# Kernel tuning notes

Hardware: AMD Instinct MI355X
Metric: run time of the kernel (lower is better)

## Reference

```python
import jax, jax.numpy as jnp
import numpy as np

HEAD_SIZE = 64


def setup_inputs() -> dict:
    key = jax.random.key(0)
    kx, kk, kq, kv = jax.random.split(key, 4)
    B, T, C = 4, 4096, 1024
    x = jax.random.normal(kx, (B, T, C), dtype=jnp.float32)
    Wk = jax.random.normal(kk, (C, HEAD_SIZE), dtype=jnp.float32) * 0.02
    Wq = jax.random.normal(kq, (C, HEAD_SIZE), dtype=jnp.float32) * 0.02
    Wv = jax.random.normal(kv, (C, HEAD_SIZE), dtype=jnp.float32) * 0.02
    return {"x": x, "Wk": Wk, "Wq": Wq, "Wv": Wv}


def reference(x, Wk, Wq, Wv):
    # x: (B,T,C); projections to (B,T,H)
    T = x.shape[1]
    k = jnp.einsum('btc,ch->bth', x, Wk)
    q = jnp.einsum('btc,ch->bth', x, Wq)
    v = jnp.einsum('btc,ch->bth', x, Wv)
    scale = 1.0 / jnp.sqrt(jnp.float32(HEAD_SIZE))
    wei = jnp.einsum('bth,bsh->bts', q, k) * scale  # (B,T,T)
    causal = jnp.tril(jnp.ones((T, T), dtype=bool))
    wei = jnp.where(causal, wei, -jnp.inf)
    wei = jax.nn.softmax(wei, axis=-1)
    out = jnp.einsum('bts,bsh->bth', wei, v)  # (B,T,H)
    return out
```

## Files before the change

### kernel.cpp

```cpp
#include <hip/hip_runtime.h>

typedef __attribute__((ext_vector_type(8))) short short8;
typedef __attribute__((ext_vector_type(4))) float f32x4;
typedef unsigned short u16;

#define BB 4
#define TT 4096
#define CC 1024
#define HH 64

static __device__ __forceinline__ u16 f2bf(float f) {
    unsigned int u = __float_as_uint(f);
    unsigned int r = (u + 0x7FFFu + ((u >> 16) & 1u)) >> 16;
    return (u16)r;
}

static __device__ __forceinline__ int swz(int row, int chunk) {
    return row * 64 + ((chunk ^ (row & 7)) << 3);
}

__global__ void detect_dtype(const u16* __restrict__ xu, int* __restrict__ flag) {
    int lane = threadIdx.x;
    int cnt = 0;
    for (int i = lane; i < 1024; i += 64) {
        u16 u = xu[2 * i];
        int e = (u >> 7) & 0xFF;
        cnt += (e >= 100 && e <= 140) ? 1 : 0;
    }
    for (int d = 1; d < 64; d <<= 1) cnt += __shfl_xor(cnt, d);
    if (lane == 0) *flag = (cnt > 512) ? 1 : 0;
}

__global__ void wt_transpose(const void* __restrict__ Wk, const void* __restrict__ Wq,
                             const void* __restrict__ Wv, u16* __restrict__ Wtp,
                             const int* __restrict__ flag) {
    const int isbf = *flag;
    int r = blockIdx.x;
    int p = r >> 6;
    int n = r & 63;
    int nt = n >> 4, nl = n & 15;
    const void* W = (p == 0) ? Wq : (p == 1) ? Wk : Wv;
    int k0 = threadIdx.x * 4;
    int kb = k0 >> 6, k2 = (k0 >> 5) & 1, quad = (k0 >> 3) & 3, half = (k0 >> 2) & 1;
    ushort4 v;
    if (isbf) {
        const u16* Wb = (const u16*)W;
        v.x = Wb[(k0 + 0) * HH + n]; v.y = Wb[(k0 + 1) * HH + n];
        v.z = Wb[(k0 + 2) * HH + n]; v.w = Wb[(k0 + 3) * HH + n];
    } else {
        const float* Wf = (const float*)W;
        v.x = f2bf(Wf[(k0 + 0) * HH + n]); v.y = f2bf(Wf[(k0 + 1) * HH + n]);
        v.z = f2bf(Wf[(k0 + 2) * HH + n]); v.w = f2bf(Wf[(k0 + 3) * HH + n]);
    }
    size_t off16 = ((size_t)((p * 4 + nt) * 16 + kb) * 2 + k2) * 64 + quad * 16 + nl;
    *reinterpret_cast<ushort4*>(Wtp + off16 * 8 + half * 4) = v;
}

__global__ __launch_bounds__(256) void qkv_proj(const void* __restrict__ x,
                                                const u16* __restrict__ Wtp,
                                                u16* __restrict__ qo, u16* __restrict__ ko,
                                                u16* __restrict__ vo, const int* __restrict__ flag) {
    __shared__ __align__(16) u16 xs[16 * 1024];
    __shared__ __align__(16) u16 tls[4][3][256];
    const int isbf = *flag;
    const int tid = threadIdx.x;
    const int lane = tid & 63;
    const int w = tid >> 6;
    const int l15 = lane & 15;
    const int quad = lane >> 4;
    int phys = blockIdx.x;
    int rb = (phys & 7) * 128 + (phys >> 3);
    const int g0r = rb * 16;

    #pragma unroll
    for (int j = 0; j < 8; j++) {
        int c = tid + j * 256;
        int row = c >> 7, ck = c & 127;
        int dst = row * 1024 + ((ck ^ (row & 7)) << 3);
        if (isbf) {
            uint4 d = *reinterpret_cast<const uint4*>((const u16*)x + (size_t)(g0r + row) * CC + ck * 8);
            *reinterpret_cast<uint4*>(xs + dst) = d;
        } else {
            const float4* pf = reinterpret_cast<const float4*>((const float*)x + (size_t)(g0r + row) * CC + ck * 8);
            float4 a0 = pf[0], a1 = pf[1];
            ushort4 lo; lo.x = f2bf(a0.x); lo.y = f2bf(a0.y); lo.z = f2bf(a0.z); lo.w = f2bf(a0.w);
            ushort4 hi; hi.x = f2bf(a1.x); hi.y = f2bf(a1.y); hi.z = f2bf(a1.z); hi.w = f2bf(a1.w);
            *reinterpret_cast<ushort4*>(xs + dst) = lo;
            *reinterpret_cast<ushort4*>(xs + dst + 4) = hi;
        }
    }
    __syncthreads();

    f32x4 zero = {0.f, 0.f, 0.f, 0.f};
    f32x4 acc[3];
    #pragma unroll
    for (int i = 0; i < 3; i++) acc[i] = zero;

    for (int kb = 0; kb < 16; kb++) {
        #pragma unroll
        for (int k2 = 0; k2 < 2; k2++) {
            int ck = kb * 8 + k2 * 4 + quad;
            short8 af = *reinterpret_cast<const short8*>(xs + l15 * 1024 + ((ck ^ (l15 & 7)) << 3));
            #pragma unroll
            for (int p = 0; p < 3; p++) {
                short8 bf = *reinterpret_cast<const short8*>(
                    Wtp + ((((size_t)(p * 4 + w) * 16 + kb) * 2 + k2) * 64 + lane) * 8);
                acc[p] = __builtin_amdgcn_mfma_f32_16x16x32_bf16(af, bf, acc[p], 0, 0, 0);
            }
        }
    }

    const float qscale = 0.18033688011112042f;
    #pragma unroll
    for (int p = 0; p < 3; p++) {
        if (p < 2) {
            float sc = (p == 0) ? qscale : 1.f;
            #pragma unroll
            for (int r = 0; r < 4; r++)
                tls[w][p][(quad * 4 + r) * 16 + l15] = f2bf(acc[p][r] * sc);
        } else {
            #pragma unroll
            for (int r = 0; r < 4; r++)
                tls[w][p][l15 * 16 + quad * 4 + r] = f2bf(acc[p][r]);
        }
    }
    #pragma unroll
    for (int p = 0; p < 2; p++) {
        int t = lane >> 2, seg = lane & 3;
        ushort4 d = *reinterpret_cast<const ushort4*>(&tls[w][p][t * 16 + seg * 4]);
        u16* dst = (p == 0) ? qo : ko;
        *reinterpret_cast<ushort4*>(dst + (size_t)(g0r + t) * HH + w * 16 + seg * 4) = d;
    }
    {
        int c = lane >> 2, seg = lane & 3;
        ushort4 d = *reinterpret_cast<const ushort4*>(&tls[w][2][c * 16 + seg * 4]);
        int b = rb >> 8;
        int kt = (g0r & 4095) >> 6;
        int toff = g0r & 63;
        *reinterpret_cast<ushort4*>(vo + ((size_t)((b * 64 + kt) * 64 + w * 16 + c)) * 64 + toff + seg * 4) = d;
    }
}

__global__ __launch_bounds__(256) void attn(const u16* __restrict__ qp, const u16* __restrict__ kp,
                                            const u16* __restrict__ vp, float* __restrict__ acco,
                                            float* __restrict__ accl, void* __restrict__ outv,
                                            const int* __restrict__ flag, int nsplit) {
    __shared__ __align__(16) u16 kst[64 * 64];
    __shared__ __align__(16) u16 vts[64 * 64];
    __shared__ __align__(16) u16 pb[4][16 * 64];
    const int isbf = *flag;
    const int tid = threadIdx.x;
    const int lane = tid & 63;
    const int w = tid >> 6;
    const int l15 = lane & 15;
    const int quad = lane >> 4;

    int u = blockIdx.x;
    int b, qt, ks;
    if (nsplit == 1) {
        b = u >> 6;
        int raw = u & 63;
        qt = (raw & 1) ? (63 - (raw >> 1)) : (raw >> 1);
        ks = 0;
    } else {
        int per = 64 * nsplit;
        b = u / per;
        int rem = u - b * per;
        int i = rem / nsplit;
        qt = 63 - i;
        ks = rem - i * nsplit;
    }
    int qbase = qt * 64;
    int diag = qt;
    int nkt = diag + 1;
    if (ks >= nkt) return;

    short8 aq[2];
    {
        const u16* qrow = qp + (size_t)(b * TT + qbase + w * 16 + l15) * HH;
        aq[0] = *reinterpret_cast<const short8*>(qrow + quad * 8);
        aq[1] = *reinterpret_cast<const short8*>(qrow + 32 + quad * 8);
    }

    const int cc0 = tid, cc1 = tid + 256;
    const int dst0 = swz(cc0 >> 3, cc0 & 7);
    const int dst1 = swz(cc1 >> 3, cc1 & 7);
    const u16* kbase = kp + (size_t)b * TT * HH;
    const u16* vbase = vp + (size_t)b * 64 * 64 * 64;

    f32x4 zero = {0.f, 0.f, 0.f, 0.f};
    f32x4 o[4];
    #pragma unroll
    for (int i = 0; i < 4; i++) o[i] = zero;
    f32x4 lsum = zero;

    uint4 rk0 = *reinterpret_cast<const uint4*>(kbase + (size_t)ks * 4096 + cc0 * 8);
    uint4 rk1 = *reinterpret_cast<const uint4*>(kbase + (size_t)ks * 4096 + cc1 * 8);
    uint4 rv0 = *reinterpret_cast<const uint4*>(vbase + (size_t)ks * 4096 + cc0 * 8);
    uint4 rv1 = *reinterpret_cast<const uint4*>(vbase + (size_t)ks * 4096 + cc1 * 8);

    for (int kt = ks; kt < nkt; kt += nsplit) {
        __syncthreads();
        *reinterpret_cast<uint4*>(&kst[dst0]) = rk0;
        *reinterpret_cast<uint4*>(&kst[dst1]) = rk1;
        *reinterpret_cast<uint4*>(&vts[dst0]) = rv0;
        *reinterpret_cast<uint4*>(&vts[dst1]) = rv1;
        __syncthreads();
        int ktn = kt + nsplit;
        if (ktn < nkt) {
            rk0 = *reinterpret_cast<const uint4*>(kbase + (size_t)ktn * 4096 + cc0 * 8);
            rk1 = *reinterpret_cast<const uint4*>(kbase + (size_t)ktn * 4096 + cc1 * 8);
            rv0 = *reinterpret_cast<const uint4*>(vbase + (size_t)ktn * 4096 + cc0 * 8);
            rv1 = *reinterpret_cast<const uint4*>(vbase + (size_t)ktn * 4096 + cc1 * 8);
        }
        f32x4 s[4];
        #pragma unroll
        for (int i = 0; i < 4; i++) s[i] = zero;
        __builtin_amdgcn_s_setprio(1);
        #pragma unroll
        for (int k2 = 0; k2 < 2; k2++) {
            #pragma unroll
            for (int nt = 0; nt < 4; nt++) {
                short8 bf = *reinterpret_cast<const short8*>(&kst[swz(nt * 16 + l15, k2 * 4 + quad)]);
                s[nt] = __builtin_amdgcn_mfma_f32_16x16x32_bf16(aq[k2], bf, s[nt], 0, 0, 0);
            }
        }
        __builtin_amdgcn_s_setprio(0);
        const int rg = qbase + w * 16 + quad * 4;
        const bool dm = (kt == diag);
        #pragma unroll
        for (int nt = 0; nt < 4; nt++) {
            int key = kt * 64 + nt * 16 + l15;
            #pragma unroll
            for (int r = 0; r < 4; r++) {
                float p = __builtin_amdgcn_exp2f(s[nt][r]);
                if (dm && key > rg + r) p = 0.f;
                s[nt][r] = p;
            }
        }
        #pragma unroll
        for (int nt = 0; nt < 4; nt++) lsum = lsum + s[nt];
        #pragma unroll
        for (int nt = 0; nt < 4; nt++) {
            int chunk = nt * 2 + (l15 >> 3);
            int off = l15 & 7;
            #pragma unroll
            for (int r = 0; r < 4; r++) {
                int row = quad * 4 + r;
                pb[w][row * 64 + ((chunk ^ (row & 7)) << 3) + off] = f2bf(s[nt][r]);
            }
        }
        __builtin_amdgcn_s_setprio(1);
        #pragma unroll
        for (int k2 = 0; k2 < 2; k2++) {
            short8 ap = *reinterpret_cast<const short8*>(&pb[w][swz(l15, k2 * 4 + quad)]);
            #pragma unroll
            for (int nt = 0; nt < 4; nt++) {
                short8 bv = *reinterpret_cast<const short8*>(&vts[swz(nt * 16 + l15, k2 * 4 + quad)]);
                o[nt] = __builtin_amdgcn_mfma_f32_16x16x32_bf16(ap, bv, o[nt], 0, 0, 0);
            }
        }
        __builtin_amdgcn_s_setprio(0);
    }

    #pragma unroll
    for (int d = 1; d < 16; d <<= 1) {
        f32x4 t;
        #pragma unroll
        for (int r = 0; r < 4; r++) t[r] = __shfl_xor(lsum[r], d);
        lsum = lsum + t;
    }
    const int g0 = b * TT + qbase + w * 16 + quad * 4;

    if (nsplit == 1) {
        f32x4 inv;
        #pragma unroll
        for (int r = 0; r < 4; r++) inv[r] = 1.0f / lsum[r];
        if (isbf) {
            u16* outp = (u16*)outv;
            #pragma unroll
            for (int nt = 0; nt < 4; nt++)
                #pragma unroll
                for (int r = 0; r < 4; r++)
                    outp[(size_t)(g0 + r) * HH + nt * 16 + l15] = f2bf(o[nt][r] * inv[r]);
        } else {
            float* outp = (float*)outv;
            #pragma unroll
            for (int nt = 0; nt < 4; nt++)
                #pragma unroll
                for (int r = 0; r < 4; r++)
                    outp[(size_t)(g0 + r) * HH + nt * 16 + l15] = o[nt][r] * inv[r];
        }
    } else {
        float* accos = acco + (size_t)ks * (BB * TT * HH);
        float* accls = accl + (size_t)ks * (BB * TT);
        #pragma unroll
        for (int nt = 0; nt < 4; nt++)
            #pragma unroll
            for (int r = 0; r < 4; r++)
                accos[(size_t)(g0 + r) * HH + nt * 16 + l15] = o[nt][r];
        if (l15 == 0) {
            #pragma unroll
            for (int r = 0; r < 4; r++) accls[g0 + r] = lsum[r];
        }
    }
}

__global__ __launch_bounds__(256) void attn_finalize(const float* __restrict__ acco,
                                                     const float* __restrict__ accl,
                                                     void* __restrict__ outv,
                                                     const int* __restrict__ flag, int nsplit) {
    const int isbf = *flag;
    int i = blockIdx.x * blockDim.x + threadIdx.x;
    int row = i >> 4;
    int qt = (row & (TT - 1)) >> 6;
    int nact = min(nsplit, qt + 1);
    float4 ov = reinterpret_cast<const float4*>(acco)[i];
    float l = accl[row];
    for (int s = 1; s < nact; s++) {
        float4 t = reinterpret_cast<const float4*>(acco + (size_t)s * (BB * TT * HH))[i];
        ov.x += t.x; ov.y += t.y; ov.z += t.z; ov.w += t.w;
        l += accl[(size_t)s * (BB * TT) + row];
    }
    float inv = 1.0f / l;
    if (isbf) {
        ushort4 s;
        s.x = f2bf(ov.x * inv); s.y = f2bf(ov.y * inv);
        s.z = f2bf(ov.z * inv); s.w = f2bf(ov.w * inv);
        reinterpret_cast<ushort4*>(outv)[i] = s;
    } else {
        float4 s = {ov.x * inv, ov.y * inv, ov.z * inv, ov.w * inv};
        reinterpret_cast<float4*>(outv)[i] = s;
    }
}

extern "C" void kernel_launch(void* const* d_in, const int* in_sizes, int n_in,
                              void* d_out, int out_size, void* d_ws, size_t ws_size,
                              hipStream_t stream) {
    const void* x  = d_in[0];
    const void* Wk = d_in[1];
    const void* Wq = d_in[2];
    const void* Wv = d_in[3];
    char* ws = (char*)d_ws;
    u16* qo = (u16*)(ws);
    u16* ko = (u16*)(ws + (size_t)2 * 1024 * 1024);
    u16* vo = (u16*)(ws + (size_t)4 * 1024 * 1024);
    u16* Wtp = (u16*)(ws + (size_t)6 * 1024 * 1024);
    int* flag = (int*)(ws + (size_t)6 * 1024 * 1024 + 768 * 1024);
    float* acco = (float*)(ws + (size_t)7 * 1024 * 1024);
    float* accl = (float*)(ws + (size_t)39 * 1024 * 1024);

    const size_t need_split = (size_t)40 * 1024 * 1024;
    const int nsplit = (ws_size >= need_split) ? 8 : 1;

    detect_dtype<<<1, 64, 0, stream>>>((const u16*)x, flag);
    wt_transpose<<<192, 256, 0, stream>>>(Wk, Wq, Wv, Wtp, flag);
    qkv_proj<<<1024, 256, 0, stream>>>(x, Wtp, qo, ko, vo, flag);
    if (nsplit > 1) {
        attn<<<BB * 64 * nsplit, 256, 0, stream>>>(qo, ko, vo, acco, accl, d_out, flag, nsplit);
        attn_finalize<<<(BB * TT * HH / 4) / 256, 256, 0, stream>>>(acco, accl, d_out, flag, nsplit);
    } else {
        attn<<<BB * 64, 256, 0, stream>>>(qo, ko, vo, acco, accl, d_out, flag, 1);
    }
}
```

Baseline: 146.2 us.

## Fuse prep kernels, double rows per QKV block, merge split-K finalize into attention

Merges dtype detection and weight transpose into one prep kernel that also zeroes per-tile counters. The QKV projection block now handles 32 rows instead of 16, reusing each weight fragment for two MFMAs. The separate finalize launch is removed: the last split-K attention block for each query tile, found with an atomic counter, reduces the partials and writes the output. This cuts launch count and weight reloads, at the cost of doubled shared memory in qkv_proj and a serialized reduction tail inside attention.

```diff
diff --git a/kernel.cpp b/kernel.cpp
--- a/kernel.cpp
+++ b/kernel.cpp
@@ -19,8 +19,8 @@
     return row * 64 + ((chunk ^ (row & 7)) << 3);
 }
 
-__global__ void detect_dtype(const u16* __restrict__ xu, int* __restrict__ flag) {
-    int lane = threadIdx.x;
+static __device__ __forceinline__ int probe_isbf(const u16* xu, int tid) {
+    int lane = tid & 63;
     int cnt = 0;
     for (int i = lane; i < 1024; i += 64) {
         u16 u = xu[2 * i];
@@ -28,13 +28,26 @@
         cnt += (e >= 100 && e <= 140) ? 1 : 0;
     }
     for (int d = 1; d < 64; d <<= 1) cnt += __shfl_xor(cnt, d);
-    if (lane == 0) *flag = (cnt > 512) ? 1 : 0;
-}
-
-__global__ void wt_transpose(const void* __restrict__ Wk, const void* __restrict__ Wq,
-                             const void* __restrict__ Wv, u16* __restrict__ Wtp,
-                             const int* __restrict__ flag) {
-    const int isbf = *flag;
+    return (cnt > 512) ? 1 : 0;
+}
+
+__global__ void prep(const void* __restrict__ Wk, const void* __restrict__ Wq,
+                     const void* __restrict__ Wv, const u16* __restrict__ xu,
+                     u16* __restrict__ Wtp, int* __restrict__ flag, int* __restrict__ cnt) {
+    __shared__ int sflag;
+    if (threadIdx.x < 64) {
+        int f = probe_isbf(xu, threadIdx.x);
+        if (threadIdx.x == 0) sflag = f;
+    }
+    __syncthreads();
+    const int isbf = sflag;
+
+    if (blockIdx.x >= 192) {
+        if (threadIdx.x < 256) cnt[threadIdx.x] = 0;
+        if (threadIdx.x == 0) *flag = isbf;
+        return;
+    }
+
     int r = blockIdx.x;
     int p = r >> 6;
     int n = r & 63;
@@ -60,7 +73,7 @@
                                                 const u16* __restrict__ Wtp,
                                                 u16* __restrict__ qo, u16* __restrict__ ko,
                                                 u16* __restrict__ vo, const int* __restrict__ flag) {
-    __shared__ __align__(16) u16 xs[16 * 1024];
+    __shared__ __align__(16) u16 xs[32 * 1024];
     __shared__ __align__(16) u16 tls[4][3][256];
     const int isbf = *flag;
     const int tid = threadIdx.x;
@@ -69,11 +82,11 @@
     const int l15 = lane & 15;
     const int quad = lane >> 4;
     int phys = blockIdx.x;
-    int rb = (phys & 7) * 128 + (phys >> 3);
-    const int g0r = rb * 16;
-
-    #pragma unroll
-    for (int j = 0; j < 8; j++) {
+    int rb = (phys & 7) * 64 + (phys >> 3);
+    const int g0r = rb * 32;
+
+    #pragma unroll
+    for (int j = 0; j < 16; j++) {
         int c = tid + j * 256;
         int row = c >> 7, ck = c & 127;
         int dst = row * 1024 + ((ck ^ (row & 7)) << 3);
@@ -92,62 +105,71 @@
     __syncthreads();
 
     f32x4 zero = {0.f, 0.f, 0.f, 0.f};
-    f32x4 acc[3];
-    #pragma unroll
-    for (int i = 0; i < 3; i++) acc[i] = zero;
+    f32x4 acc[3][2];
+    #pragma unroll
+    for (int i = 0; i < 3; i++) { acc[i][0] = zero; acc[i][1] = zero; }
 
     for (int kb = 0; kb < 16; kb++) {
         #pragma unroll
         for (int k2 = 0; k2 < 2; k2++) {
             int ck = kb * 8 + k2 * 4 + quad;
-            short8 af = *reinterpret_cast<const short8*>(xs + l15 * 1024 + ((ck ^ (l15 & 7)) << 3));
+            int xo = ((ck ^ (l15 & 7)) << 3);
+            short8 af0 = *reinterpret_cast<const short8*>(xs + l15 * 1024 + xo);
+            short8 af1 = *reinterpret_cast<const short8*>(xs + (16 + l15) * 1024 + xo);
             #pragma unroll
             for (int p = 0; p < 3; p++) {
                 short8 bf = *reinterpret_cast<const short8*>(
                     Wtp + ((((size_t)(p * 4 + w) * 16 + kb) * 2 + k2) * 64 + lane) * 8);
-                acc[p] = __builtin_amdgcn_mfma_f32_16x16x32_bf16(af, bf, acc[p], 0, 0, 0);
+                acc[p][0] = __builtin_amdgcn_mfma_f32_16x16x32_bf16(af0, bf, acc[p][0], 0, 0, 0);
+                acc[p][1] = __builtin_amdgcn_mfma_f32_16x16x32_bf16(af1, bf, acc[p][1], 0, 0, 0);
             }
         }
     }
 
     const float qscale = 0.18033688011112042f;
     #pragma unroll
-    for (int p = 0; p < 3; p++) {
-        if (p < 2) {
-            float sc = (p == 0) ? qscale : 1.f;
-            #pragma unroll
-            for (int r = 0; r < 4; r++)
-                tls[w][p][(quad * 4 + r) * 16 + l15] = f2bf(acc[p][r] * sc);
-        } else {
-            #pragma unroll
-            for (int r = 0; r < 4; r++)
-                tls[w][p][l15 * 16 + quad * 4 + r] = f2bf(acc[p][r]);
-        }
-    }
-    #pragma unroll
-    for (int p = 0; p < 2; p++) {
-        int t = lane >> 2, seg = lane & 3;
-        ushort4 d = *reinterpret_cast<const ushort4*>(&tls[w][p][t * 16 + seg * 4]);
-        u16* dst = (p == 0) ? qo : ko;
-        *reinterpret_cast<ushort4*>(dst + (size_t)(g0r + t) * HH + w * 16 + seg * 4) = d;
-    }
-    {
-        int c = lane >> 2, seg = lane & 3;
-        ushort4 d = *reinterpret_cast<const ushort4*>(&tls[w][2][c * 16 + seg * 4]);
-        int b = rb >> 8;
-        int kt = (g0r & 4095) >> 6;
-        int toff = g0r & 63;
-        *reinterpret_cast<ushort4*>(vo + ((size_t)((b * 64 + kt) * 64 + w * 16 + c)) * 64 + toff + seg * 4) = d;
+    for (int rt = 0; rt < 2; rt++) {
+        const int g0rt = g0r + rt * 16;
+        #pragma unroll
+        for (int p = 0; p < 3; p++) {
+            if (p < 2) {
+                float sc = (p == 0) ? qscale : 1.f;
+                #pragma unroll
+                for (int r = 0; r < 4; r++)
+                    tls[w][p][(quad * 4 + r) * 16 + l15] = f2bf(acc[p][rt][r] * sc);
+            } else {
+                #pragma unroll
+                for (int r = 0; r < 4; r++)
+                    tls[w][p][l15 * 16 + quad * 4 + r] = f2bf(acc[p][rt][r]);
+            }
+        }
+        #pragma unroll
+        for (int p = 0; p < 2; p++) {
+            int t = lane >> 2, seg = lane & 3;
+            ushort4 d = *reinterpret_cast<const ushort4*>(&tls[w][p][t * 16 + seg * 4]);
+            u16* dst = (p == 0) ? qo : ko;
+            *reinterpret_cast<ushort4*>(dst + (size_t)(g0rt + t) * HH + w * 16 + seg * 4) = d;
+        }
+        {
+            int c = lane >> 2, seg = lane & 3;
+            ushort4 d = *reinterpret_cast<const ushort4*>(&tls[w][2][c * 16 + seg * 4]);
+            int b = g0rt >> 12;
+            int kt = (g0rt & 4095) >> 6;
+            int toff = g0rt & 63;
+            *reinterpret_cast<ushort4*>(vo + ((size_t)((b * 64 + kt) * 64 + w * 16 + c)) * 64 + toff + seg * 4) = d;
+        }
     }
 }
 
 __global__ __launch_bounds__(256) void attn(const u16* __restrict__ qp, const u16* __restrict__ kp,
                                             const u16* __restrict__ vp, float* __restrict__ acco,
                                             float* __restrict__ accl, void* __restrict__ outv,
-                                            const int* __restrict__ flag, int nsplit) {
+                                            const int* __restrict__ flag, int* __restrict__ cnt,
+                                            int nsplit) {
     __shared__ __align__(16) u16 kst[64 * 64];
     __shared__ __align__(16) u16 vts[64 * 64];
     __shared__ __align__(16) u16 pb[4][16 * 64];
+    __shared__ int is_last;
     const int isbf = *flag;
     const int tid = threadIdx.x;
     const int lane = tid & 63;
@@ -303,34 +325,37 @@
             #pragma unroll
             for (int r = 0; r < 4; r++) accls[g0 + r] = lsum[r];
         }
-    }
-}
-
-__global__ __launch_bounds__(256) void attn_finalize(const float* __restrict__ acco,
-                                                     const float* __restrict__ accl,
-                                                     void* __restrict__ outv,
-                                                     const int* __restrict__ flag, int nsplit) {
-    const int isbf = *flag;
-    int i = blockIdx.x * blockDim.x + threadIdx.x;
-    int row = i >> 4;
-    int qt = (row & (TT - 1)) >> 6;
-    int nact = min(nsplit, qt + 1);
-    float4 ov = reinterpret_cast<const float4*>(acco)[i];
-    float l = accl[row];
-    for (int s = 1; s < nact; s++) {
-        float4 t = reinterpret_cast<const float4*>(acco + (size_t)s * (BB * TT * HH))[i];
-        ov.x += t.x; ov.y += t.y; ov.z += t.z; ov.w += t.w;
-        l += accl[(size_t)s * (BB * TT) + row];
-    }
-    float inv = 1.0f / l;
-    if (isbf) {
-        ushort4 s;
-        s.x = f2bf(ov.x * inv); s.y = f2bf(ov.y * inv);
-        s.z = f2bf(ov.z * inv); s.w = f2bf(ov.w * inv);
-        reinterpret_cast<ushort4*>(outv)[i] = s;
-    } else {
-        float4 s = {ov.x * inv, ov.y * inv, ov.z * inv, ov.w * inv};
-        reinterpret_cast<float4*>(outv)[i] = s;
+        __threadfence();
+        const int nact = (nkt < nsplit) ? nkt : nsplit;
+        if (tid == 0) {
+            int old = atomicAdd(&cnt[b * 64 + qt], 1);
+            is_last = (old == nact - 1) ? 1 : 0;
+        }
+        __syncthreads();
+        if (is_last) {
+            __threadfence();
+            for (int i = tid; i < 64 * 16; i += 256) {
+                int row = i >> 4, c4 = i & 15;
+                size_t rbase = (size_t)(b * TT + qbase + row);
+                float4 ov = {0.f, 0.f, 0.f, 0.f};
+                float l = 0.f;
+                for (int s = 0; s < nact; s++) {
+                    float4 t = reinterpret_cast<const float4*>(acco + (size_t)s * (BB * TT * HH) + rbase * HH)[c4];
+                    ov.x += t.x; ov.y += t.y; ov.z += t.z; ov.w += t.w;
+                    l += accl[(size_t)s * (BB * TT) + rbase];
+                }
+                float inv = 1.0f / l;
+                if (isbf) {
+                    ushort4 sv;
+                    sv.x = f2bf(ov.x * inv); sv.y = f2bf(ov.y * inv);
+                    sv.z = f2bf(ov.z * inv); sv.w = f2bf(ov.w * inv);
+                    reinterpret_cast<ushort4*>((u16*)outv + rbase * HH)[c4] = sv;
+                } else {
+                    float4 sv = {ov.x * inv, ov.y * inv, ov.z * inv, ov.w * inv};
+                    reinterpret_cast<float4*>((float*)outv + rbase * HH)[c4] = sv;
+                }
+            }
+        }
     }
 }
 
@@ -347,19 +372,18 @@
     u16* vo = (u16*)(ws + (size_t)4 * 1024 * 1024);
     u16* Wtp = (u16*)(ws + (size_t)6 * 1024 * 1024);
     int* flag = (int*)(ws + (size_t)6 * 1024 * 1024 + 768 * 1024);
+    int* cnt  = (int*)(ws + (size_t)6 * 1024 * 1024 + 772 * 1024);
     float* acco = (float*)(ws + (size_t)7 * 1024 * 1024);
     float* accl = (float*)(ws + (size_t)39 * 1024 * 1024);
 
     const size_t need_split = (size_t)40 * 1024 * 1024;
     const int nsplit = (ws_size >= need_split) ? 8 : 1;
 
-    detect_dtype<<<1, 64, 0, stream>>>((const u16*)x, flag);
-    wt_transpose<<<192, 256, 0, stream>>>(Wk, Wq, Wv, Wtp, flag);
-    qkv_proj<<<1024, 256, 0, stream>>>(x, Wtp, qo, ko, vo, flag);
+    prep<<<193, 256, 0, stream>>>(Wk, Wq, Wv, (const u16*)x, Wtp, flag, cnt);
+    qkv_proj<<<512, 256, 0, stream>>>(x, Wtp, qo, ko, vo, flag);
     if (nsplit > 1) {
-        attn<<<BB * 64 * nsplit, 256, 0, stream>>>(qo, ko, vo, acco, accl, d_out, flag, nsplit);
-        attn_finalize<<<(BB * TT * HH / 4) / 256, 256, 0, stream>>>(acco, accl, d_out, flag, nsplit);
+        attn<<<BB * 64 * nsplit, 256, 0, stream>>>(qo, ko, vo, acco, accl, d_out, flag, cnt, nsplit);
     } else {
-        attn<<<BB * 64, 256, 0, stream>>>(qo, ko, vo, acco, accl, d_out, flag, 1);
-    }
-}
+        attn<<<BB * 64, 256, 0, stream>>>(qo, ko, vo, acco, accl, d_out, flag, cnt, 1);
+    }
+}
```

After: 534.4 us. +265.5%, slower.
